# Performance work log

Hardware: AMD Instinct MI355X
Metric: run time of the kernel (lower is better)

The kernel has to match this reference:

```python
import jax, jax.numpy as jnp
import numpy as np

B, LQ, LK, E, HID, H = 4, 1024, 2048, 512, 512, 8


def _ln(x, g, b, eps=1e-5):
    mu = jnp.mean(x, -1, keepdims=True)
    var = jnp.mean((x - mu) ** 2, -1, keepdims=True)
    return (x - mu) * jax.lax.rsqrt(var + eps) * g + b


def _mha(q_in, k_in, v_in, Wq, bq, Wk, bk, Wv, bv, Wo, bo, nheads, q_valid, k_valid):
    # torch nn.MultiheadAttention (batch_first, eval/dropout=0) math
    Bq, Lq, Em = q_in.shape
    Lk = k_in.shape[1]
    hd = Em // nheads
    q = (q_in @ Wq.T + bq).reshape(Bq, Lq, nheads, hd)
    k = (k_in @ Wk.T + bk).reshape(Bq, Lk, nheads, hd)
    v = (v_in @ Wv.T + bv).reshape(Bq, Lk, nheads, hd)
    scale = 1.0 / np.sqrt(hd).astype(np.float32)
    s = jnp.einsum('bqhd,bkhd->bhqk', q, k) * scale
    if k_valid is not None:
        # valid query rows may only attend to valid key columns
        s = jnp.where(k_valid[:, None, None, :], s, jnp.finfo(s.dtype).min)
    w = jax.nn.softmax(s, axis=-1)
    # rows beyond a sample's length are fully masked in the torch nested path
    # (softmax -> NaN, later nan_to_num'd to 0); we zero them directly.
    w = jnp.where(q_valid[:, None, :, None], w, 0.0)
    o = jnp.einsum('bhqk,bkhd->bqhd', w, v).reshape(Bq, Lq, Em)
    return o @ Wo.T + bo, jnp.mean(w, axis=1)  # weights averaged over heads


def setup_inputs() -> dict:
    key = jax.random.key(0)
    ks = jax.random.split(key, 32)
    p = lambda i, shape: 0.02 * jax.random.normal(ks[i], shape, dtype=jnp.float32)
    inp = {
        'queries': jax.random.normal(ks[0], (B, LQ, E), dtype=jnp.float32),
        'keys': jax.random.normal(ks[1], (B, LK, E), dtype=jnp.float32),
        'q_len': jax.random.randint(ks[2], (B,), 1, LQ + 1),
        # cross-attention params
        'cWq': p(3, (E, E)), 'cbq': jnp.zeros((E,)),
        'cWk': p(4, (E, E)), 'cbk': jnp.zeros((E,)),
        'cWv': p(5, (E, E)), 'cbv': jnp.zeros((E,)),
        'cWo': p(6, (E, E)), 'cbo': jnp.zeros((E,)),
        # self-attention params
        'sWq': p(7, (HID, HID)), 'sbq': jnp.zeros((HID,)),
        'sWk': p(8, (HID, HID)), 'sbk': jnp.zeros((HID,)),
        'sWv': p(9, (HID, HID)), 'sbv': jnp.zeros((HID,)),
        'sWo': p(10, (HID, HID)), 'sbo': jnp.zeros((HID,)),
        # ffn + norms
        'Wf': p(11, (HID, E)), 'bf': jnp.zeros((HID,)),
        'g_cross': jnp.ones((E,)), 'b_cross': jnp.zeros((E,)),
        'g_ffn': jnp.ones((HID,)), 'b_ffn': jnp.zeros((HID,)),
        'g_self': jnp.ones((HID,)), 'b_self': jnp.zeros((HID,)),
    }
    return inp


def reference(queries, keys, q_len,
              cWq, cbq, cWk, cbk, cWv, cbv, cWo, cbo,
              sWq, sbq, sWk, sbk, sWv, sbv, sWo, sbo,
              Wf, bf, g_cross, b_cross, g_ffn, b_ffn, g_self, b_self):
    valid = jnp.arange(LQ)[None, :] < q_len[:, None]  # [B, LQ] ragged lengths
    q = jnp.where(valid[..., None], queries, 0.0)     # nested -> padded with 0
    # cross attention: valid rows attend to ALL keys (per the nested mask)
    cross, weights = _mha(q, keys, keys, cWq, cbq, cWk, cbk, cWv, cbv, cWo, cbo,
                          H, valid, None)
    q = _ln(jax.nn.silu(cross + q), g_cross, b_cross)
    f = q @ Wf.T + bf
    q = _ln(jax.nn.silu(q + f), g_ffn, b_ffn)  # q_dim == hidden_dim branch
    q = jnp.where(valid[..., None], q, 0.0)    # torch.nan_to_num on padded rows
    # self attention: valid rows attend only to valid rows of the same sample
    so, _ = _mha(q, q, q, sWq, sbq, sWk, sbk, sWv, sbv, sWo, sbo, H, valid, valid)
    q = _ln(jax.nn.silu(q + so), g_self, b_self)
    q = jnp.where(valid[..., None], q, 0.0)    # padded rows discarded by unbind
    return q, weights
```

## Files before the change

### kernel.cpp

```cpp
#include <hip/hip_runtime.h>

#define BB 4
#define SLQ 1024
#define SLK 2048
#define EE 512
#define HH 8
#define HD 64

typedef unsigned short u16;
typedef __attribute__((ext_vector_type(8))) short s16x8;
typedef __attribute__((ext_vector_type(4))) float f32x4;

__device__ __forceinline__ float bf2f(u16 u) {
  union { unsigned int i; float f; } v; v.i = ((unsigned int)u) << 16; return v.f;
}
__device__ __forceinline__ u16 f2bf(float f) {
  union { float f; unsigned int i; } v; v.f = f;
  unsigned int i = v.i;
  return (u16)((i + 0x7fffu + ((i >> 16) & 1u)) >> 16);
}

__device__ __forceinline__ void async16(const u16* g, u16* l) {
  __builtin_amdgcn_global_load_lds(
      (const __attribute__((address_space(1))) unsigned int*)g,
// ... 9 lines not shown
             const int* __restrict__ qlen)
{
  constexpr int WTM = BM / 2, WTN = BN / 2;
  constexpr int MI = WTM / 16, NI = WTN / 16;
  constexpr int EPAD = WTN + 8;
  constexpr int SM1 = (BM + BN) * 32;
  constexpr int SM2 = (MODE == 0) ? 4 * WTM * EPAD : 0;
  constexpr int SM = (SM1 > SM2) ? SM1 : SM2;

  const int z = blockIdx.z;
  const int tileM = blockIdx.y * BM;
  const int tileN = blockIdx.x * BN;

  if (SKIPQ == 1) { if (tileM >= qlen[z >> 3]) return; }
  if (SKIPQ == 2) { int b = tileM >> 10; if ((tileM & 1023) >= qlen[b]) return; }

  __shared__ __align__(16) u16 smem[SM];
  u16* ldsA = smem;
  u16* ldsB = smem + BM * 32;

  const int t = threadIdx.x;
  const int lane = t & 63;
  const int wave = t >> 6;
  const int waveM = wave >> 1;
  const int waveN = wave & 1;
  const int lm = lane & 15;
  const int kg = lane >> 4;

  const u16* Ab = A + (long)z * sAz + (long)tileM * lda;
  const u16* Bb = Bm + (long)z * sBz + (long)tileN * ldb;

  f32x4 acc[MI][NI];
#pragma unroll
  for (int i = 0; i < MI; ++i)
#pragma unroll
    for (int j = 0; j < NI; ++j) acc[i][j] = (f32x4){0.f, 0.f, 0.f, 0.f};

  for (int kt = 0; kt < K; kt += 32) {
    __syncthreads();
#pragma unroll
    for (int i = 0; i < (BM * 4) / 256; ++i) {
      int c = i * 256 + t;
      async16(Ab + (long)(c >> 2) * lda + kt + (c & 3) * 8, ldsA + (c - lane) * 8);
    }
#pragma unroll
    for (int i = 0; i < (BN * 4) / 256; ++i) {
      int c = i * 256 + t;
      async16(Bb + (long)(c >> 2) * ldb + kt + (c & 3) * 8, ldsB + (c - lane) * 8);
    }
    __syncthreads();

    s16x8 aF[MI], bF[NI];
#pragma unroll
    for (int i = 0; i < MI; ++i)
      aF[i] = *(const s16x8*)&ldsA[(waveM * WTM + i * 16 + lm) * 32 + kg * 8];
#pragma unroll
    for (int j = 0; j < NI; ++j)
      bF[j] = *(const s16x8*)&ldsB[(waveN * WTN + j * 16 + lm) * 32 + kg * 8];
#pragma unroll
    for (int i = 0; i < MI; ++i)
#pragma unroll
      for (int j = 0; j < NI; ++j)
        acc[i][j] = __builtin_amdgcn_mfma_f32_16x16x32_bf16(aF[i], bF[j], acc[i][j], 0, 0, 0);
  }

  if (MODE == 0) {
    u16* ep = smem + wave * (WTM * EPAD);
    __syncthreads();
#pragma unroll
    for (int i = 0; i < MI; ++i)
#pragma unroll
      for (int j = 0; j < NI; ++j) {
        int n = waveN * WTN + j * 16 + lm;
        float bv = bias ? bias[tileN + n] : 0.0f;
#pragma unroll
        for (int r = 0; r < 4; ++r)
          ep[(i * 16 + kg * 4 + r) * EPAD + j * 16 + lm] = f2bf(acc[i][j][r] * alpha + bv);
      }
    const long Crow = (long)z * sCz + (long)(tileM + waveM * WTM) * ldc + tileN + waveN * WTN;
#pragma unroll
    for (int it = 0; it < (WTM * WTN) / 512; ++it) {
      int idx = it * 64 + lane;
      int row = idx / (WTN / 8), seg = idx % (WTN / 8);
      *(uint4*)&C[Crow + (long)row * ldc + seg * 8] =
          *(const uint4*)&ep[row * EPAD + seg * 8];
    }
  } else {
#pragma unroll
    for (int j = 0; j < NI; ++j) {
      int n = tileN + waveN * WTN + j * 16 + lm;
      float bv = bias ? bias[n] : 0.0f;
#pragma unroll
      for (int i = 0; i < MI; ++i) {
#pragma unroll
        for (int r = 0; r < 4; ++r) {
          int m = tileM + waveM * WTM + i * 16 + kg * 4 + r;
          float v = acc[i][j][r] * alpha + bv;
          int b = m / Lsub, l = m - b * Lsub;
          int h = n >> 6, d = n & 63;
          C[(((long)(b * HH + h) * Lsub + l) << 6) + d] = f2bf(v);
        }
      }
    }
  }
}

template<int BM, int BN, int SKIPQ, int NPROJ>
// ... 73 lines not shown
      float bv = bias[n];
#pragma unroll
      for (int i = 0; i < MI; ++i)
#pragma unroll
        for (int r = 0; r < 4; ++r) {
          int m = tileM + waveM * WTM + i * 16 + kg * 4 + r;
          int b = m / Lsub, l = m - b * Lsub;
          int h = n >> 6, d = n & 63;
          C[(((long)(b * HH + h) * Lsub + l) << 6) + d] = f2bf(acc[i][j][r] + bv);
        }
    }
  } else {
    constexpr int PAD = BM + 8;
    const int bb = tileM / Lsub;
    const int l0 = tileM - bb * Lsub;
#pragma unroll
    for (int c = 0; c < BN / 32; ++c) {
      __syncthreads();
#pragma unroll
      for (int j = 0; j < NI; ++j) {
        int nloc = waveN * WTN + j * 16 + lm;
        if (nloc >= c * 32 && nloc < c * 32 + 32) {
          int nl = nloc - c * 32;
          float bv = bias[tileN + nloc];
#pragma unroll
          for (int i = 0; i < MI; ++i)
#pragma unroll
            for (int r = 0; r < 4; ++r) {
              int mm = waveM * WTM + i * 16 + kg * 4 + r;
              smem[nl * PAD + mm] = f2bf(acc[i][j][r] + bv);
            }
        }
      }
      __syncthreads();
#pragma unroll
      for (int v = 0; v < (32 * BM) / (256 * 8); ++v) {
        int idx = v * 256 + t;
        int nl = idx / (BM / 8), m8 = idx % (BM / 8);
        int n = tileN + c * 32 + nl;
        int h = n >> 6, d = n & 63;
        *(uint4*)&C[((long)(bb * HH + h) * HD + d) * Lsub + l0 + m8 * 8] =
            *(const uint4*)&smem[nl * PAD + m8 * 8];
      }
    }
  }
}

__global__ __launch_bounds__(256, 3)
void cross_flash_chunk(const u16* __restrict__ Qc, const u16* __restrict__ Kc,
                       const u16* __restrict__ Vt, u16* __restrict__ Opart,
                       float2* __restrict__ ml, const int* __restrict__ qlen)
{
  const int lin = blockIdx.x;
  const int lid = (lin & 7) * 256 + (lin >> 3);
  const int qt = lid & 15;
  const int bh = (lid >> 4) & 31;
  const int ck = lid >> 9;
  const int b = bh >> 3;
  if (qt * 64 >= qlen[b]) return;

  __shared__ __align__(16) u16 Kt[128 * 72];
  __shared__ __align__(16) u16 Vl[64 * 136];

  const int t = threadIdx.x, lane = t & 63, w = t >> 6;
  const int col = lane & 15, quad = lane >> 4;

  const u16* Qb = Qc + (long)bh * SLQ * HD;
  const u16* Kb = Kc + (long)bh * SLK * HD;
  const u16* Vb = Vt + (long)bh * HD * SLK;

  s16x8 aQ[2];
#pragma unroll
  for (int kk = 0; kk < 2; ++kk)
    aQ[kk] = *(const s16x8*)(Qb + (long)(qt * 64 + w * 16 + col) * HD + kk * 32 + quad * 8);

  f32x4 O[4];
#pragma unroll
  for (int n = 0; n < 4; ++n) O[n] = (f32x4){0.f, 0.f, 0.f, 0.f};
  float mr = -1e30f, lr = 0.f;

  u16* Pw = Kt + w * (16 * 136);

  const int krow = t >> 3, kcol = (t & 7) * 8;
  const int vrow = t >> 4, vcol = (t & 15) * 8;

  uint4 kr0, kr1, kr2, kr3, vr0, vr1, vr2, vr3;
  {
    const int kb = ck * 512;
    kr0 = *(const uint4*)(Kb + (long)(kb + krow) * HD + kcol);
    kr1 = *(const uint4*)(Kb + (long)(kb + krow + 32) * HD + kcol);
    kr2 = *(const uint4*)(Kb + (long)(kb + krow + 64) * HD + kcol);
    kr3 = *(const uint4*)(Kb + (long)(kb + krow + 96) * HD + kcol);
    vr0 = *(const uint4*)(Vb + (long)(vrow) * SLK + kb + vcol);
    vr1 = *(const uint4*)(Vb + (long)(vrow + 16) * SLK + kb + vcol);
    vr2 = *(const uint4*)(Vb + (long)(vrow + 32) * SLK + kb + vcol);
    vr3 = *(const uint4*)(Vb + (long)(vrow + 48) * SLK + kb + vcol);
  }

#pragma unroll
  for (int kt = 0; kt < 4; ++kt) {
    __syncthreads();
    *(uint4*)&Kt[(krow) * 72 + kcol] = kr0;
    *(uint4*)&Kt[(krow + 32) * 72 + kcol] = kr1;
    *(uint4*)&Kt[(krow + 64) * 72 + kcol] = kr2;
    *(uint4*)&Kt[(krow + 96) * 72 + kcol] = kr3;
    *(uint4*)&Vl[(vrow) * 136 + vcol] = vr0;
    *(uint4*)&Vl[(vrow + 16) * 136 + vcol] = vr1;
    *(uint4*)&Vl[(vrow + 32) * 136 + vcol] = vr2;
    *(uint4*)&Vl[(vrow + 48) * 136 + vcol] = vr3;
    if (kt < 3) {
      const int kb = ck * 512 + (kt + 1) * 128;
      kr0 = *(const uint4*)(Kb + (long)(kb + krow) * HD + kcol);
      kr1 = *(const uint4*)(Kb + (long)(kb + krow + 32) * HD + kcol);
      kr2 = *(const uint4*)(Kb + (long)(kb + krow + 64) * HD + kcol);
      kr3 = *(const uint4*)(Kb + (long)(kb + krow + 96) * HD + kcol);
      vr0 = *(const uint4*)(Vb + (long)(vrow) * SLK + kb + vcol);
      vr1 = *(const uint4*)(Vb + (long)(vrow + 16) * SLK + kb + vcol);
      vr2 = *(const uint4*)(Vb + (long)(vrow + 32) * SLK + kb + vcol);
      vr3 = *(const uint4*)(Vb + (long)(vrow + 48) * SLK + kb + vcol);
    }
    __syncthreads();

    f32x4 s[8];
#pragma unroll
    for (int j = 0; j < 8; ++j) s[j] = (f32x4){0.f, 0.f, 0.f, 0.f};
#pragma unroll
    for (int j = 0; j < 8; ++j)
#pragma unroll
      for (int kk = 0; kk < 2; ++kk) {
        s16x8 bK = *(const s16x8*)&Kt[(j * 16 + col) * 72 + kk * 32 + quad * 8];
        s[j] = __builtin_amdgcn_mfma_f32_16x16x32_bf16(bK, aQ[kk], s[j], 0, 0, 0);
      }
#pragma unroll
    for (int j = 0; j < 8; ++j)
#pragma unroll
      for (int r = 0; r < 4; ++r)
        s[j][r] *= 0.125f;

    __syncthreads();

    float mj[8];
#pragma unroll
    for (int j = 0; j < 8; ++j)
      mj[j] = fmaxf(fmaxf(s[j][0], s[j][1]), fmaxf(s[j][2], s[j][3]));
    float tm = fmaxf(fmaxf(fmaxf(mj[0], mj[1]), fmaxf(mj[2], mj[3])),
                     fmaxf(fmaxf(mj[4], mj[5]), fmaxf(mj[6], mj[7])));
    tm = fmaxf(tm, __shfl_xor(tm, 16));
    tm = fmaxf(tm, __shfl_xor(tm, 32));
    float mnew = fmaxf(mr, tm);
    float alpha = __expf(mr - mnew);
    mr = mnew;
    float psj[8];
#pragma unroll
    for (int j = 0; j < 8; ++j) {
      float p0 = __expf(s[j][0] - mnew);
      float p1 = __expf(s[j][1] - mnew);
      float p2 = __expf(s[j][2] - mnew);
      float p3 = __expf(s[j][3] - mnew);
      psj[j] = (p0 + p1) + (p2 + p3);
      unsigned int lo = (unsigned int)f2bf(p0) | ((unsigned int)f2bf(p1) << 16);
      unsigned int hi = (unsigned int)f2bf(p2) | ((unsigned int)f2bf(p3) << 16);
      *(uint2*)&Pw[col * 136 + j * 16 + quad * 4] = (uint2){lo, hi};
    }
    float ps = ((psj[0] + psj[1]) + (psj[2] + psj[3])) +
               ((psj[4] + psj[5]) + (psj[6] + psj[7]));
    ps += __shfl_xor(ps, 16);
    ps += __shfl_xor(ps, 32);
    lr = lr * alpha + ps;

    float a0 = __shfl(alpha, quad * 4 + 0);
    float a1 = __shfl(alpha, quad * 4 + 1);
    float a2 = __shfl(alpha, quad * 4 + 2);
    float a3 = __shfl(alpha, quad * 4 + 3);
#pragma unroll
    for (int n = 0; n < 4; ++n) {
      O[n][0] *= a0; O[n][1] *= a1; O[n][2] *= a2; O[n][3] *= a3;
    }
#pragma unroll
    for (int kk = 0; kk < 4; ++kk) {
      s16x8 aP = *(const s16x8*)&Pw[col * 136 + kk * 32 + quad * 8];
#pragma unroll
      for (int n = 0; n < 4; ++n) {
        s16x8 bV = *(const s16x8*)&Vl[(n * 16 + col) * 136 + kk * 32 + quad * 8];
        O[n] = __builtin_amdgcn_mfma_f32_16x16x32_bf16(aP, bV, O[n], 0, 0, 0);
      }
    }
  }

#pragma unroll
  for (int r = 0; r < 4; ++r) {
    int q = qt * 64 + w * 16 + quad * 4 + r;
    long gq = (long)bh * SLQ + q;
#pragma unroll
    for (int n = 0; n < 4; ++n)
      Opart[(gq * 4 + ck) * 64 + n * 16 + col] = f2bf(O[n][r]);
  }
  if (quad == 0) {
    int q = qt * 64 + w * 16 + col;
    ml[((long)bh * SLQ + q) * 4 + ck] = (float2){mr, lr};
  }
}

__global__ __launch_bounds__(256)
void cross_combine(const u16* __restrict__ Opart, const float2* __restrict__ ml,
                   u16* __restrict__ attn, float2* __restrict__ stat,
                   const int* __restrict__ qlen)
{
  int gr = blockIdx.x * 16 + (threadIdx.x >> 4);
  int bh = gr >> 10, q = gr & 1023;
  int b = bh >> 3, h = bh & 7;
  if (q >= qlen[b]) return;
  int d = (threadIdx.x & 15) * 4;
  long base = (long)gr * 4;
  float M = -1e30f;
#pragma unroll
  for (int c = 0; c < 4; ++c) M = fmaxf(M, ml[base + c].x);
  float L = 0.f;
  float ax = 0.f, ay = 0.f, az = 0.f, aw = 0.f;
#pragma unroll
  for (int c = 0; c < 4; ++c) {
    float2 st = ml[base + c];
    float wgt = __expf(st.x - M);
    L += st.y * wgt;
    const u16* p = Opart + (base + c) * 64 + d;
    ax += bf2f(p[0]) * wgt; ay += bf2f(p[1]) * wgt;
    az += bf2f(p[2]) * wgt; aw += bf2f(p[3]) * wgt;
  }
  if (d == 0) stat[gr] = (float2){M, L};
  float inv = 1.0f / L;
  unsigned int lo = (unsigned int)f2bf(ax * inv) | ((unsigned int)f2bf(ay * inv) << 16);
  unsigned int hi = (unsigned int)f2bf(az * inv) | ((unsigned int)f2bf(aw * inv) << 16);
  *(uint2*)&attn[((long)b * SLQ + q) * EE + h * HD + d] = (uint2){lo, hi};
}

__global__ __launch_bounds__(256, 4)
void wmean_recompute(const u16* __restrict__ Qc, const u16* __restrict__ Kc,
                     const float2* __restrict__ stat, float* __restrict__ outw,
                     const int* __restrict__ qlen)
{
  const int kt = blockIdx.x;
  const int qt = blockIdx.y;
  const int b  = blockIdx.z;
  const int qn = qlen[b];
  const int q0 = qt * 64;
  const int t = threadIdx.x, lane = t & 63, w = t >> 6;
  const int col = lane & 15, quad = lane >> 4;

  float* wr = outw + ((long)b * SLQ + q0) * SLK + kt * 128;

  if (q0 >= qn) {
    float4 z = {0.f, 0.f, 0.f, 0.f};
    for (int i = t; i < 64 * 32; i += 256) {
// ... 29 lines not shown
    *(uint4*)&Kl[(krow + 64) * 72 + kcol] = kr2;
    *(uint4*)&Kl[(krow + 96) * 72 + kcol] = kr3;
    if (h < 7) {
      const u16* Kn = Kbase + (long)(h + 1) * SLK * HD;
      kr0 = *(const uint4*)(Kn + (long)(krow) * HD + kcol);
      kr1 = *(const uint4*)(Kn + (long)(krow + 32) * HD + kcol);
      kr2 = *(const uint4*)(Kn + (long)(krow + 64) * HD + kcol);
      kr3 = *(const uint4*)(Kn + (long)(krow + 96) * HD + kcol);
    }
    const u16* Qb = Qc + ((long)bh * SLQ + qw) * HD;
    s16x8 aQ0 = *(const s16x8*)(Qb + col * HD + quad * 8);
    s16x8 aQ1 = *(const s16x8*)(Qb + col * HD + 32 + quad * 8);
    float m_[4], il_[4];
#pragma unroll
    for (int r = 0; r < 4; ++r) {
      float2 st = stat[(long)bh * SLQ + qw + quad * 4 + r];
      m_[r] = st.x; il_[r] = 0.125f / st.y;
    }
    __syncthreads();

    f32x4 s[8];
#pragma unroll
    for (int j = 0; j < 8; ++j) s[j] = (f32x4){0.f, 0.f, 0.f, 0.f};
#pragma unroll
    for (int j = 0; j < 8; ++j) {
      s16x8 bK0 = *(const s16x8*)&Kl[(j * 16 + col) * 72 + quad * 8];
      s16x8 bK1 = *(const s16x8*)&Kl[(j * 16 + col) * 72 + 32 + quad * 8];
      s[j] = __builtin_amdgcn_mfma_f32_16x16x32_bf16(aQ0, bK0, s[j], 0, 0, 0);
      s[j] = __builtin_amdgcn_mfma_f32_16x16x32_bf16(aQ1, bK1, s[j], 0, 0, 0);
    }
#pragma unroll
    for (int j = 0; j < 8; ++j)
#pragma unroll
      for (int r = 0; r < 4; ++r)
        acc[j][r] += __expf(s[j][r] * 0.125f - m_[r]) * il_[r];
  }

#pragma unroll
  for (int r = 0; r < 4; ++r) {
    int row = w * 16 + quad * 4 + r;
    bool v = (q0 + row) < qn;
#pragma unroll
    for (int j = 0; j < 8; ++j)
      wr[(long)row * SLK + j * 16 + col] = v ? acc[j][r] : 0.f;
  }
}

__global__ __launch_bounds__(256, 3)
void self_flash_chunk(const u16* __restrict__ Qc, const u16* __restrict__ Kc,
                      const u16* __restrict__ Vt, u16* __restrict__ Opart,
                      float2* __restrict__ ml, const int* __restrict__ qlen)
{
  const int lin = blockIdx.x;
  const int lid = (lin & 7) * 256 + (lin >> 3);
  const int qt = lid & 15;
  const int bh = (lid >> 4) & 31;
  const int ck = lid >> 9;
  const int b = bh >> 3;
  const int kmax = qlen[b];
  if (qt * 64 >= kmax || ck * 256 >= kmax) return;

  __shared__ __align__(16) u16 Kt[128 * 72];
  __shared__ __align__(16) u16 Vl[64 * 136];

  const int t = threadIdx.x, lane = t & 63, w = t >> 6;
  const int col = lane & 15, quad = lane >> 4;

  const u16* Qb = Qc + (long)bh * SLQ * HD;
  const u16* Kb = Kc + (long)bh * SLQ * HD;
  const u16* Vb = Vt + (long)bh * HD * SLQ;

  s16x8 aQ[2];
#pragma unroll
  for (int kk = 0; kk < 2; ++kk)
    aQ[kk] = *(const s16x8*)(Qb + (long)(qt * 64 + w * 16 + col) * HD + kk * 32 + quad * 8);

  f32x4 O[4];
#pragma unroll
  for (int n = 0; n < 4; ++n) O[n] = (f32x4){0.f, 0.f, 0.f, 0.f};
  float mr = -1e30f, lr = 0.f;

  u16* Pw = Kt + w * (16 * 136);

  const int krow = t >> 3, kcol = (t & 7) * 8;
  const int vrow = t >> 4, vcol = (t & 15) * 8;

  uint4 kr0, kr1, kr2, kr3, vr0, vr1, vr2, vr3;
  {
    const int kb = ck * 256;
    kr0 = *(const uint4*)(Kb + (long)(kb + krow) * HD + kcol);
    kr1 = *(const uint4*)(Kb + (long)(kb + krow + 32) * HD + kcol);
    kr2 = *(const uint4*)(Kb + (long)(kb + krow + 64) * HD + kcol);
    kr3 = *(const uint4*)(Kb + (long)(kb + krow + 96) * HD + kcol);
    vr0 = *(const uint4*)(Vb + (long)(vrow) * SLQ + kb + vcol);
    vr1 = *(const uint4*)(Vb + (long)(vrow + 16) * SLQ + kb + vcol);
    vr2 = *(const uint4*)(Vb + (long)(vrow + 32) * SLQ + kb + vcol);
    vr3 = *(const uint4*)(Vb + (long)(vrow + 48) * SLQ + kb + vcol);
  }

#pragma unroll
  for (int kt = 0; kt < 2; ++kt) {
    const int k0 = ck * 256 + kt * 128;
    if (k0 >= kmax) break;
    __syncthreads();
    *(uint4*)&Kt[(krow) * 72 + kcol] = kr0;
    *(uint4*)&Kt[(krow + 32) * 72 + kcol] = kr1;
    *(uint4*)&Kt[(krow + 64) * 72 + kcol] = kr2;
    *(uint4*)&Kt[(krow + 96) * 72 + kcol] = kr3;
    *(uint4*)&Vl[(vrow) * 136 + vcol] = vr0;
    *(uint4*)&Vl[(vrow + 16) * 136 + vcol] = vr1;
    *(uint4*)&Vl[(vrow + 32) * 136 + vcol] = vr2;
    *(uint4*)&Vl[(vrow + 48) * 136 + vcol] = vr3;
    if (kt < 1) {
      const int kb = ck * 256 + 128;
      kr0 = *(const uint4*)(Kb + (long)(kb + krow) * HD + kcol);
      kr1 = *(const uint4*)(Kb + (long)(kb + krow + 32) * HD + kcol);
      kr2 = *(const uint4*)(Kb + (long)(kb + krow + 64) * HD + kcol);
      kr3 = *(const uint4*)(Kb + (long)(kb + krow + 96) * HD + kcol);
      vr0 = *(const uint4*)(Vb + (long)(vrow) * SLQ + kb + vcol);
      vr1 = *(const uint4*)(Vb + (long)(vrow + 16) * SLQ + kb + vcol);
      vr2 = *(const uint4*)(Vb + (long)(vrow + 32) * SLQ + kb + vcol);
      vr3 = *(const uint4*)(Vb + (long)(vrow + 48) * SLQ + kb + vcol);
    }
    __syncthreads();

    f32x4 s[8];
#pragma unroll
    for (int j = 0; j < 8; ++j) s[j] = (f32x4){0.f, 0.f, 0.f, 0.f};
#pragma unroll
    for (int j = 0; j < 8; ++j)
#pragma unroll
      for (int kk = 0; kk < 2; ++kk) {
        s16x8 bK = *(const s16x8*)&Kt[(j * 16 + col) * 72 + kk * 32 + quad * 8];
        s[j] = __builtin_amdgcn_mfma_f32_16x16x32_bf16(bK, aQ[kk], s[j], 0, 0, 0);
      }
#pragma unroll
    for (int j = 0; j < 8; ++j)
#pragma unroll
      for (int r = 0; r < 4; ++r) {
        bool ok = (k0 + j * 16 + quad * 4 + r) < kmax;
        s[j][r] = ok ? s[j][r] * 0.125f : -1e30f;
      }

    __syncthreads();

    float mj[8];
#pragma unroll
    for (int j = 0; j < 8; ++j)
      mj[j] = fmaxf(fmaxf(s[j][0], s[j][1]), fmaxf(s[j][2], s[j][3]));
    float tm = fmaxf(fmaxf(fmaxf(mj[0], mj[1]), fmaxf(mj[2], mj[3])),
                     fmaxf(fmaxf(mj[4], mj[5]), fmaxf(mj[6], mj[7])));
    tm = fmaxf(tm, __shfl_xor(tm, 16));
    tm = fmaxf(tm, __shfl_xor(tm, 32));
    float mnew = fmaxf(mr, tm);
    float alpha = __expf(mr - mnew);
    mr = mnew;
    float psj[8];
#pragma unroll
    for (int j = 0; j < 8; ++j) {
      float p0 = __expf(s[j][0] - mnew);
      float p1 = __expf(s[j][1] - mnew);
      float p2 = __expf(s[j][2] - mnew);
      float p3 = __expf(s[j][3] - mnew);
      psj[j] = (p0 + p1) + (p2 + p3);
      unsigned int lo = (unsigned int)f2bf(p0) | ((unsigned int)f2bf(p1) << 16);
      unsigned int hi = (unsigned int)f2bf(p2) | ((unsigned int)f2bf(p3) << 16);
      *(uint2*)&Pw[col * 136 + j * 16 + quad * 4] = (uint2){lo, hi};
    }
    float ps = ((psj[0] + psj[1]) + (psj[2] + psj[3])) +
               ((psj[4] + psj[5]) + (psj[6] + psj[7]));
    ps += __shfl_xor(ps, 16);
    ps += __shfl_xor(ps, 32);
    lr = lr * alpha + ps;

    float a0 = __shfl(alpha, quad * 4 + 0);
    float a1 = __shfl(alpha, quad * 4 + 1);
    float a2 = __shfl(alpha, quad * 4 + 2);
    float a3 = __shfl(alpha, quad * 4 + 3);
#pragma unroll
    for (int n = 0; n < 4; ++n) {
      O[n][0] *= a0; O[n][1] *= a1; O[n][2] *= a2; O[n][3] *= a3;
    }
#pragma unroll
    for (int kk = 0; kk < 4; ++kk) {
      s16x8 aP = *(const s16x8*)&Pw[col * 136 + kk * 32 + quad * 8];
#pragma unroll
      for (int n = 0; n < 4; ++n) {
        s16x8 bV = *(const s16x8*)&Vl[(n * 16 + col) * 136 + kk * 32 + quad * 8];
        O[n] = __builtin_amdgcn_mfma_f32_16x16x32_bf16(aP, bV, O[n], 0, 0, 0);
      }
    }
  }

#pragma unroll
  for (int r = 0; r < 4; ++r) {
    int q = qt * 64 + w * 16 + quad * 4 + r;
    long gq = (long)bh * SLQ + q;
#pragma unroll
    for (int n = 0; n < 4; ++n)
      Opart[(gq * 4 + ck) * 64 + n * 16 + col] = f2bf(O[n][r]);
  }
  if (quad == 0) {
    int q = qt * 64 + w * 16 + col;
    ml[((long)bh * SLQ + q) * 4 + ck] = (float2){mr, lr};
  }
}

__global__ __launch_bounds__(256)
void self_combine(const u16* __restrict__ Opart, const float2* __restrict__ ml,
                  u16* __restrict__ attn, const int* __restrict__ qlen)
{
  int gr = blockIdx.x * 16 + (threadIdx.x >> 4);
  int bh = gr >> 10, q = gr & 1023;
  int b = bh >> 3, h = bh & 7;
  int kmax = qlen[b];
  if (q >= kmax) return;
  int NC = (kmax + 255) >> 8;
  int d = (threadIdx.x & 15) * 4;
  long base = (long)gr * 4;
  float M = -1e30f;
  for (int c = 0; c < NC; ++c) M = fmaxf(M, ml[base + c].x);
  float L = 0.f;
  float ax = 0.f, ay = 0.f, az = 0.f, aw = 0.f;
  for (int c = 0; c < NC; ++c) {
    float2 st = ml[base + c];
    float wgt = __expf(st.x - M);
    L += st.y * wgt;
    const u16* p = Opart + (base + c) * 64 + d;
    ax += bf2f(p[0]) * wgt; ay += bf2f(p[1]) * wgt;
    az += bf2f(p[2]) * wgt; aw += bf2f(p[3]) * wgt;
  }
  float inv = 1.0f / L;
  unsigned int lo = (unsigned int)f2bf(ax * inv) | ((unsigned int)f2bf(ay * inv) << 16);
  unsigned int hi = (unsigned int)f2bf(az * inv) | ((unsigned int)f2bf(aw * inv) << 16);
  *(uint2*)&attn[((long)b * SLQ + q) * EE + h * HD + d] = (uint2){lo, hi};
}

__global__ __launch_bounds__(256)
void cvt_all(const float* __restrict__ queries, const float* __restrict__ keys,
             const int* __restrict__ qlen,
             const float* w0, const float* w1, const float* w2, const float* w3,
             const float* w4, const float* w5, const float* w6, const float* w7,
             const float* w8,
             u16* __restrict__ q0, u16* __restrict__ keysb, u16* __restrict__ Wb) {
  int blk = blockIdx.x;
  int t = threadIdx.x;
  const float* src;
  u16* dst;
  long off;
  bool mask = false;
  int b = 0, q = 0;
  if (blk < 1024) {
    off = (long)blk * 2048 + t * 8;
    int row = (int)(off >> 9);
    b = row >> 10; q = row & 1023;
    mask = true;
    src = queries; dst = q0;
// ... 81 lines not shown
  const float* cWk = (const float*)d_in[5],  *cbk = (const float*)d_in[6];
  const float* cWv = (const float*)d_in[7],  *cbv = (const float*)d_in[8];
  const float* cWo = (const float*)d_in[9],  *cbo = (const float*)d_in[10];
  const float* sWq = (const float*)d_in[11], *sbq = (const float*)d_in[12];
  const float* sWk = (const float*)d_in[13], *sbk = (const float*)d_in[14];
  const float* sWv = (const float*)d_in[15], *sbv = (const float*)d_in[16];
  const float* sWo = (const float*)d_in[17], *sbo = (const float*)d_in[18];
  const float* Wf  = (const float*)d_in[19], *bfb = (const float*)d_in[20];
  const float* g_cross = (const float*)d_in[21], *b_cross = (const float*)d_in[22];
  const float* g_ffn   = (const float*)d_in[23], *b_ffn   = (const float*)d_in[24];
  const float* g_self  = (const float*)d_in[25], *b_self  = (const float*)d_in[26];

  float* out_q = (float*)d_out;
  float* out_w = out_q + (long)BB * SLQ * EE;

  u16* ws = (u16*)d_ws;
  u16* S     = ws;
  u16* Qc    = S   + (long)BB * HH * SLQ * SLK;
  u16* Kc    = Qc  + (long)BB * HH * SLQ * HD;
  u16* Vt    = Kc  + (long)BB * HH * SLK * HD;
  u16* q0    = Vt  + (long)BB * HH * SLK * HD;
  u16* keysb = q0  + (long)BB * SLQ * EE;
  u16* attn  = keysb + (long)BB * SLK * EE;
  u16* proj  = attn + (long)BB * SLQ * EE;
  u16* q1    = proj + (long)BB * SLQ * EE;
  u16* fbuf  = q1  + (long)BB * SLQ * EE;
  u16* q2    = fbuf + (long)BB * SLQ * EE;
  u16* Wb    = q2  + (long)BB * SLQ * EE;
  const long WSLOT = (long)EE * EE;
  u16*    Cpb  = Wb + 9 * WSLOT;
  float2* stat = (float2*)(Cpb + 8388608);

  float2* mlC = (float2*)(S + 33554432);

  u16*    OpS = S;
  float2* mlS = (float2*)(S + 8388608);

  u16* bWq = Wb + 0 * WSLOT; u16* bWk = Wb + 1 * WSLOT; u16* bWv = Wb + 2 * WSLOT;
  u16* bWo = Wb + 3 * WSLOT; u16* bsWq = Wb + 4 * WSLOT; u16* bsWk = Wb + 5 * WSLOT;
  u16* bsWv = Wb + 6 * WSLOT; u16* bsWo = Wb + 7 * WSLOT; u16* bWf = Wb + 8 * WSLOT;

  dim3 blk(256);
  const int MQ = BB * SLQ;
  const int MK = BB * SLK;

  cvt_all<<<dim3(3072 + 9 * 128), blk, 0, stream>>>(
      queries, keys, qlen, cWq, cWk, cWv, cWo, sWq, sWk, sWv, sWo, Wf, q0, keysb, Wb);

  gemm_nt<64, 64, 1, 2><<<dim3(EE / 64, MQ / 64, 1), blk, 0, stream>>>(
      q0, bWq, cbq, Qc, MQ, EE, EE, EE, EE, 0, 0, 0, 0, 1.0f, SLQ, qlen);
  gemm_proj<64, 64, 0, 2><<<dim3(EE / 64, MK / 64, 2), blk, 0, stream>>>(
      keysb, bWk, bWv, nullptr, cbk, cbv, nullptr, Kc, Vt, nullptr, MK, EE, SLK, qlen);

  cross_flash_chunk<<<dim3(2048), blk, 0, stream>>>(Qc, Kc, Vt, Cpb, mlC, qlen);
  cross_combine<<<dim3(2048), blk, 0, stream>>>(Cpb, mlC, attn, stat, qlen);
  wmean_recompute<<<dim3(16, 16, BB), blk, 0, stream>>>(Qc, Kc, stat, out_w, qlen);

  gemm_nt<64, 64, 0, 2><<<dim3(EE / 64, MQ / 64, 1), blk, 0, stream>>>(
      attn, bWo, cbo, proj, MQ, EE, EE, EE, EE, EE, 0, 0, 0, 1.0f, SLQ, qlen);

  silu_ln_kernel<0><<<dim3(MQ), blk, 0, stream>>>(proj, q0, g_cross, b_cross, qlen, q1, 2);

  gemm_nt<64, 64, 0, 2><<<dim3(EE / 64, MQ / 64, 1), blk, 0, stream>>>(
      q1, bWf, bfb, fbuf, MQ, EE, EE, EE, EE, EE, 0, 0, 0, 1.0f, SLQ, qlen);

  silu_ln_kernel<0><<<dim3(MQ), blk, 0, stream>>>(q1, fbuf, g_ffn, b_ffn, qlen, q2, 1);

  gemm_proj<64, 64, 2, 3><<<dim3(EE / 64, MQ / 64, 3), blk, 0, stream>>>(
      q2, bsWq, bsWk, bsWv, sbq, sbk, sbv, Qc, Kc, Vt, MQ, EE, SLQ, qlen);

  self_flash_chunk<<<dim3(2048), blk, 0, stream>>>(Qc, Kc, Vt, OpS, mlS, qlen);
  self_combine<<<dim3(2048), blk, 0, stream>>>(OpS, mlS, attn, qlen);

  gemm_nt<64, 64, 0, 2><<<dim3(EE / 64, MQ / 64, 1), blk, 0, stream>>>(
      attn, bsWo, sbo, proj, MQ, EE, EE, EE, EE, EE, 0, 0, 0, 1.0f, SLQ, qlen);

  silu_ln_kernel<1><<<dim3(MQ), blk, 0, stream>>>(q2, proj, g_self, b_self, qlen, out_q, 1);
}
```

Before: 296.4 us.

## Process two query tiles per flash-attention block to reuse staged K/V tiles

Both the cross and self flash-attention chunk kernels now handle 128 query rows per block (two 64-row groups A and B) instead of 64, so each K/V tile staged into LDS serves twice as many queries and the grid is halved. P gets its own LDS buffer instead of aliasing the K tile, which removes one barrier per tile but raises LDS use and may lower occupancy. The key-tile and group loops are set to unroll 1, which limits register pressure from the doubled accumulators but may cost scheduling freedom. A second group is skipped when it lies beyond the sequence length.

```diff
diff --git a/kernel.cpp b/kernel.cpp
--- a/kernel.cpp
+++ b/kernel.cpp
@@ -85,7 +85,7 @@
 
     s16x8 aF[MI], bF[NI];
 #pragma unroll
-    for (int i = 0; i < MI; ++i)
+  for (int i = 0; i < MI; ++i)
       aF[i] = *(const s16x8*)&ldsA[(waveM * WTM + i * 16 + lm) * 32 + kg * 8];
 #pragma unroll
     for (int j = 0; j < NI; ++j)
@@ -265,15 +265,18 @@
                        float2* __restrict__ ml, const int* __restrict__ qlen)
 {
   const int lin = blockIdx.x;
-  const int lid = (lin & 7) * 256 + (lin >> 3);
-  const int qt = lid & 15;
-  const int bh = (lid >> 4) & 31;
-  const int ck = lid >> 9;
+  const int lid = (lin & 7) * 128 + (lin >> 3);
+  const int qt = lid & 7;
+  const int bh = (lid >> 3) & 31;
+  const int ck = lid >> 8;
   const int b = bh >> 3;
-  if (qt * 64 >= qlen[b]) return;
+  const int qn = qlen[b];
+  if (qt * 128 >= qn) return;
+  const bool doB = (qt * 128 + 64) < qn;
 
   __shared__ __align__(16) u16 Kt[128 * 72];
   __shared__ __align__(16) u16 Vl[64 * 136];
+  __shared__ __align__(16) u16 Pl[4 * 16 * 136];
 
   const int t = threadIdx.x, lane = t & 63, w = t >> 6;
   const int col = lane & 15, quad = lane >> 4;
@@ -282,17 +285,22 @@
   const u16* Kb = Kc + (long)bh * SLK * HD;
   const u16* Vb = Vt + (long)bh * HD * SLK;
 
-  s16x8 aQ[2];
-#pragma unroll
-  for (int kk = 0; kk < 2; ++kk)
-    aQ[kk] = *(const s16x8*)(Qb + (long)(qt * 64 + w * 16 + col) * HD + kk * 32 + quad * 8);
-
-  f32x4 O[4];
-#pragma unroll
-  for (int n = 0; n < 4; ++n) O[n] = (f32x4){0.f, 0.f, 0.f, 0.f};
-  float mr = -1e30f, lr = 0.f;
-
-  u16* Pw = Kt + w * (16 * 136);
+  const int qA = qt * 128 + w * 16 + col;
+  const int qB = qA + 64;
+  s16x8 aQA0 = *(const s16x8*)(Qb + (long)qA * HD + quad * 8);
+  s16x8 aQA1 = *(const s16x8*)(Qb + (long)qA * HD + 32 + quad * 8);
+  s16x8 aQB0 = *(const s16x8*)(Qb + (long)qB * HD + quad * 8);
+  s16x8 aQB1 = *(const s16x8*)(Qb + (long)qB * HD + 32 + quad * 8);
+
+  f32x4 OA[4], OB[4];
+#pragma unroll
+  for (int n = 0; n < 4; ++n) {
+    OA[n] = (f32x4){0.f, 0.f, 0.f, 0.f};
+    OB[n] = (f32x4){0.f, 0.f, 0.f, 0.f};
+  }
+  float mrA = -1e30f, lrA = 0.f, mrB = -1e30f, lrB = 0.f;
+
+  u16* Pw = Pl + w * (16 * 136);
 
   const int krow = t >> 3, kcol = (t & 7) * 8;
   const int vrow = t >> 4, vcol = (t & 15) * 8;
@@ -310,7 +318,7 @@
     vr3 = *(const uint4*)(Vb + (long)(vrow + 48) * SLK + kb + vcol);
   }
 
-#pragma unroll
+#pragma unroll 1
   for (int kt = 0; kt < 4; ++kt) {
     __syncthreads();
     *(uint4*)&Kt[(krow) * 72 + kcol] = kr0;
@@ -334,83 +342,118 @@
     }
     __syncthreads();
 
-    f32x4 s[8];
-#pragma unroll
-    for (int j = 0; j < 8; ++j) s[j] = (f32x4){0.f, 0.f, 0.f, 0.f};
-#pragma unroll
-    for (int j = 0; j < 8; ++j)
-#pragma unroll
-      for (int kk = 0; kk < 2; ++kk) {
-        s16x8 bK = *(const s16x8*)&Kt[(j * 16 + col) * 72 + kk * 32 + quad * 8];
-        s[j] = __builtin_amdgcn_mfma_f32_16x16x32_bf16(bK, aQ[kk], s[j], 0, 0, 0);
-      }
-#pragma unroll
-    for (int j = 0; j < 8; ++j)
-#pragma unroll
-      for (int r = 0; r < 4; ++r)
-        s[j][r] *= 0.125f;
-
-    __syncthreads();
-
-    float mj[8];
-#pragma unroll
-    for (int j = 0; j < 8; ++j)
-      mj[j] = fmaxf(fmaxf(s[j][0], s[j][1]), fmaxf(s[j][2], s[j][3]));
-    float tm = fmaxf(fmaxf(fmaxf(mj[0], mj[1]), fmaxf(mj[2], mj[3])),
-                     fmaxf(fmaxf(mj[4], mj[5]), fmaxf(mj[6], mj[7])));
-    tm = fmaxf(tm, __shfl_xor(tm, 16));
-    tm = fmaxf(tm, __shfl_xor(tm, 32));
-    float mnew = fmaxf(mr, tm);
-    float alpha = __expf(mr - mnew);
-    mr = mnew;
-    float psj[8];
-#pragma unroll
-    for (int j = 0; j < 8; ++j) {
-      float p0 = __expf(s[j][0] - mnew);
-      float p1 = __expf(s[j][1] - mnew);
-      float p2 = __expf(s[j][2] - mnew);
-      float p3 = __expf(s[j][3] - mnew);
-      psj[j] = (p0 + p1) + (p2 + p3);
-      unsigned int lo = (unsigned int)f2bf(p0) | ((unsigned int)f2bf(p1) << 16);
-      unsigned int hi = (unsigned int)f2bf(p2) | ((unsigned int)f2bf(p3) << 16);
-      *(uint2*)&Pw[col * 136 + j * 16 + quad * 4] = (uint2){lo, hi};
-    }
-    float ps = ((psj[0] + psj[1]) + (psj[2] + psj[3])) +
-               ((psj[4] + psj[5]) + (psj[6] + psj[7]));
-    ps += __shfl_xor(ps, 16);
-    ps += __shfl_xor(ps, 32);
-    lr = lr * alpha + ps;
-
-    float a0 = __shfl(alpha, quad * 4 + 0);
-    float a1 = __shfl(alpha, quad * 4 + 1);
-    float a2 = __shfl(alpha, quad * 4 + 2);
-    float a3 = __shfl(alpha, quad * 4 + 3);
-#pragma unroll
-    for (int n = 0; n < 4; ++n) {
-      O[n][0] *= a0; O[n][1] *= a1; O[n][2] *= a2; O[n][3] *= a3;
-    }
-#pragma unroll
-    for (int kk = 0; kk < 4; ++kk) {
-      s16x8 aP = *(const s16x8*)&Pw[col * 136 + kk * 32 + quad * 8];
-#pragma unroll
-      for (int n = 0; n < 4; ++n) {
-        s16x8 bV = *(const s16x8*)&Vl[(n * 16 + col) * 136 + kk * 32 + quad * 8];
-        O[n] = __builtin_amdgcn_mfma_f32_16x16x32_bf16(aP, bV, O[n], 0, 0, 0);
+#pragma unroll 1
+    for (int g = 0; g < 2; ++g) {
+      if (g == 1 && !doB) break;
+      const s16x8 aQ0 = (g == 0) ? aQA0 : aQB0;
+      const s16x8 aQ1 = (g == 0) ? aQA1 : aQB1;
+      float mr = (g == 0) ? mrA : mrB;
+      float lr = (g == 0) ? lrA : lrB;
+
+      f32x4 s[8];
+#pragma unroll
+      for (int j = 0; j < 8; ++j) s[j] = (f32x4){0.f, 0.f, 0.f, 0.f};
+#pragma unroll
+      for (int j = 0; j < 8; ++j) {
+        s16x8 bK0 = *(const s16x8*)&Kt[(j * 16 + col) * 72 + quad * 8];
+        s16x8 bK1 = *(const s16x8*)&Kt[(j * 16 + col) * 72 + 32 + quad * 8];
+        s[j] = __builtin_amdgcn_mfma_f32_16x16x32_bf16(bK0, aQ0, s[j], 0, 0, 0);
+        s[j] = __builtin_amdgcn_mfma_f32_16x16x32_bf16(bK1, aQ1, s[j], 0, 0, 0);
+      }
+#pragma unroll
+      for (int j = 0; j < 8; ++j)
+#pragma unroll
+        for (int r = 0; r < 4; ++r)
+          s[j][r] *= 0.125f;
+
+      float mj[8];
+#pragma unroll
+      for (int j = 0; j < 8; ++j)
+        mj[j] = fmaxf(fmaxf(s[j][0], s[j][1]), fmaxf(s[j][2], s[j][3]));
+      float tm = fmaxf(fmaxf(fmaxf(mj[0], mj[1]), fmaxf(mj[2], mj[3])),
+                       fmaxf(fmaxf(mj[4], mj[5]), fmaxf(mj[6], mj[7])));
+      tm = fmaxf(tm, __shfl_xor(tm, 16));
+      tm = fmaxf(tm, __shfl_xor(tm, 32));
+      float mnew = fmaxf(mr, tm);
+      float alpha = __expf(mr - mnew);
+      mr = mnew;
+      float psj[8];
+#pragma unroll
+      for (int j = 0; j < 8; ++j) {
+        float p0 = __expf(s[j][0] - mnew);
+        float p1 = __expf(s[j][1] - mnew);
+        float p2 = __expf(s[j][2] - mnew);
+        float p3 = __expf(s[j][3] - mnew);
+        psj[j] = (p0 + p1) + (p2 + p3);
+        unsigned int lo = (unsigned int)f2bf(p0) | ((unsigned int)f2bf(p1) << 16);
+        unsigned int hi = (unsigned int)f2bf(p2) | ((unsigned int)f2bf(p3) << 16);
+        *(uint2*)&Pw[col * 136 + j * 16 + quad * 4] = (uint2){lo, hi};
+      }
+      float ps = ((psj[0] + psj[1]) + (psj[2] + psj[3])) +
+                 ((psj[4] + psj[5]) + (psj[6] + psj[7]));
+      ps += __shfl_xor(ps, 16);
+      ps += __shfl_xor(ps, 32);
+      lr = lr * alpha + ps;
+
+      float a0 = __shfl(alpha, quad * 4 + 0);
+      float a1 = __shfl(alpha, quad * 4 + 1);
+      float a2 = __shfl(alpha, quad * 4 + 2);
+      float a3 = __shfl(alpha, quad * 4 + 3);
+      if (g == 0) {
+#pragma unroll
+        for (int n = 0; n < 4; ++n) {
+          OA[n][0] *= a0; OA[n][1] *= a1; OA[n][2] *= a2; OA[n][3] *= a3;
+        }
+#pragma unroll
+        for (int kk = 0; kk < 4; ++kk) {
+          s16x8 aP = *(const s16x8*)&Pw[col * 136 + kk * 32 + quad * 8];
+#pragma unroll
+          for (int n = 0; n < 4; ++n) {
+            s16x8 bV = *(const s16x8*)&Vl[(n * 16 + col) * 136 + kk * 32 + quad * 8];
+            OA[n] = __builtin_amdgcn_mfma_f32_16x16x32_bf16(aP, bV, OA[n], 0, 0, 0);
+          }
+        }
+        mrA = mr; lrA = lr;
+      } else {
+#pragma unroll
+        for (int n = 0; n < 4; ++n) {
+          OB[n][0] *= a0; OB[n][1] *= a1; OB[n][2] *= a2; OB[n][3] *= a3;
+        }
+#pragma unroll
+        for (int kk = 0; kk < 4; ++kk) {
+          s16x8 aP = *(const s16x8*)&Pw[col * 136 + kk * 32 + quad * 8];
+#pragma unroll
+          for (int n = 0; n < 4; ++n) {
+            s16x8 bV = *(const s16x8*)&Vl[(n * 16 + col) * 136 + kk * 32 + quad * 8];
+            OB[n] = __builtin_amdgcn_mfma_f32_16x16x32_bf16(aP, bV, OB[n], 0, 0, 0);
+          }
+        }
+        mrB = mr; lrB = lr;
       }
     }
   }
 
 #pragma unroll
   for (int r = 0; r < 4; ++r) {
-    int q = qt * 64 + w * 16 + quad * 4 + r;
+    int q = qt * 128 + w * 16 + quad * 4 + r;
     long gq = (long)bh * SLQ + q;
 #pragma unroll
     for (int n = 0; n < 4; ++n)
-      Opart[(gq * 4 + ck) * 64 + n * 16 + col] = f2bf(O[n][r]);
-  }
-  if (quad == 0) {
-    int q = qt * 64 + w * 16 + col;
-    ml[((long)bh * SLQ + q) * 4 + ck] = (float2){mr, lr};
+      Opart[(gq * 4 + ck) * 64 + n * 16 + col] = f2bf(OA[n][r]);
+  }
+  if (quad == 0)
+    ml[((long)bh * SLQ + qA) * 4 + ck] = (float2){mrA, lrA};
+  if (doB) {
+#pragma unroll
+    for (int r = 0; r < 4; ++r) {
+      int q = qt * 128 + 64 + w * 16 + quad * 4 + r;
+      long gq = (long)bh * SLQ + q;
+#pragma unroll
+      for (int n = 0; n < 4; ++n)
+        Opart[(gq * 4 + ck) * 64 + n * 16 + col] = f2bf(OB[n][r]);
+    }
+    if (quad == 0)
+      ml[((long)bh * SLQ + qB) * 4 + ck] = (float2){mrB, lrB};
   }
 }
 
@@ -546,16 +589,18 @@
                       float2* __restrict__ ml, const int* __restrict__ qlen)
 {
   const int lin = blockIdx.x;
-  const int lid = (lin & 7) * 256 + (lin >> 3);
-  const int qt = lid & 15;
-  const int bh = (lid >> 4) & 31;
-  const int ck = lid >> 9;
+  const int lid = (lin & 7) * 128 + (lin >> 3);
+  const int qt = lid & 7;
+  const int bh = (lid >> 3) & 31;
+  const int ck = lid >> 8;
   const int b = bh >> 3;
   const int kmax = qlen[b];
-  if (qt * 64 >= kmax || ck * 256 >= kmax) return;
+  if (qt * 128 >= kmax || ck * 256 >= kmax) return;
+  const bool doB = (qt * 128 + 64) < kmax;
 
   __shared__ __align__(16) u16 Kt[128 * 72];
   __shared__ __align__(16) u16 Vl[64 * 136];
+  __shared__ __align__(16) u16 Pl[4 * 16 * 136];
 
   const int t = threadIdx.x, lane = t & 63, w = t >> 6;
   const int col = lane & 15, quad = lane >> 4;
@@ -564,17 +609,22 @@
   const u16* Kb = Kc + (long)bh * SLQ * HD;
   const u16* Vb = Vt + (long)bh * HD * SLQ;
 
-  s16x8 aQ[2];
-#pragma unroll
-  for (int kk = 0; kk < 2; ++kk)
-    aQ[kk] = *(const s16x8*)(Qb + (long)(qt * 64 + w * 16 + col) * HD + kk * 32 + quad * 8);
-
-  f32x4 O[4];
-#pragma unroll
-  for (int n = 0; n < 4; ++n) O[n] = (f32x4){0.f, 0.f, 0.f, 0.f};
-  float mr = -1e30f, lr = 0.f;
-
-  u16* Pw = Kt + w * (16 * 136);
+  const int qA = qt * 128 + w * 16 + col;
+  const int qB = qA + 64;
+  s16x8 aQA0 = *(const s16x8*)(Qb + (long)qA * HD + quad * 8);
+  s16x8 aQA1 = *(const s16x8*)(Qb + (long)qA * HD + 32 + quad * 8);
+  s16x8 aQB0 = *(const s16x8*)(Qb + (long)qB * HD + quad * 8);
+  s16x8 aQB1 = *(const s16x8*)(Qb + (long)qB * HD + 32 + quad * 8);
+
+  f32x4 OA[4], OB[4];
+#pragma unroll
+  for (int n = 0; n < 4; ++n) {
+    OA[n] = (f32x4){0.f, 0.f, 0.f, 0.f};
+    OB[n] = (f32x4){0.f, 0.f, 0.f, 0.f};
+  }
+  float mrA = -1e30f, lrA = 0.f, mrB = -1e30f, lrB = 0.f;
+
+  u16* Pw = Pl + w * (16 * 136);
 
   const int krow = t >> 3, kcol = (t & 7) * 8;
   const int vrow = t >> 4, vcol = (t & 15) * 8;
@@ -592,7 +642,7 @@
     vr3 = *(const uint4*)(Vb + (long)(vrow + 48) * SLQ + kb + vcol);
   }
 
-#pragma unroll
+#pragma unroll 1
   for (int kt = 0; kt < 2; ++kt) {
     const int k0 = ck * 256 + kt * 128;
     if (k0 >= kmax) break;
@@ -618,85 +668,120 @@
     }
     __syncthreads();
 
-    f32x4 s[8];
-#pragma unroll
-    for (int j = 0; j < 8; ++j) s[j] = (f32x4){0.f, 0.f, 0.f, 0.f};
-#pragma unroll
-    for (int j = 0; j < 8; ++j)
-#pragma unroll
-      for (int kk = 0; kk < 2; ++kk) {
-        s16x8 bK = *(const s16x8*)&Kt[(j * 16 + col) * 72 + kk * 32 + quad * 8];
-        s[j] = __builtin_amdgcn_mfma_f32_16x16x32_bf16(bK, aQ[kk], s[j], 0, 0, 0);
-      }
-#pragma unroll
-    for (int j = 0; j < 8; ++j)
-#pragma unroll
-      for (int r = 0; r < 4; ++r) {
-        bool ok = (k0 + j * 16 + quad * 4 + r) < kmax;
-        s[j][r] = ok ? s[j][r] * 0.125f : -1e30f;
-      }
-
-    __syncthreads();
-
-    float mj[8];
-#pragma unroll
-    for (int j = 0; j < 8; ++j)
-      mj[j] = fmaxf(fmaxf(s[j][0], s[j][1]), fmaxf(s[j][2], s[j][3]));
-    float tm = fmaxf(fmaxf(fmaxf(mj[0], mj[1]), fmaxf(mj[2], mj[3])),
-                     fmaxf(fmaxf(mj[4], mj[5]), fmaxf(mj[6], mj[7])));
-    tm = fmaxf(tm, __shfl_xor(tm, 16));
-    tm = fmaxf(tm, __shfl_xor(tm, 32));
-    float mnew = fmaxf(mr, tm);
-    float alpha = __expf(mr - mnew);
-    mr = mnew;
-    float psj[8];
-#pragma unroll
-    for (int j = 0; j < 8; ++j) {
-      float p0 = __expf(s[j][0] - mnew);
-      float p1 = __expf(s[j][1] - mnew);
-      float p2 = __expf(s[j][2] - mnew);
-      float p3 = __expf(s[j][3] - mnew);
-      psj[j] = (p0 + p1) + (p2 + p3);
-      unsigned int lo = (unsigned int)f2bf(p0) | ((unsigned int)f2bf(p1) << 16);
-      unsigned int hi = (unsigned int)f2bf(p2) | ((unsigned int)f2bf(p3) << 16);
-      *(uint2*)&Pw[col * 136 + j * 16 + quad * 4] = (uint2){lo, hi};
-    }
-    float ps = ((psj[0] + psj[1]) + (psj[2] + psj[3])) +
-               ((psj[4] + psj[5]) + (psj[6] + psj[7]));
-    ps += __shfl_xor(ps, 16);
-    ps += __shfl_xor(ps, 32);
-    lr = lr * alpha + ps;
-
-    float a0 = __shfl(alpha, quad * 4 + 0);
-    float a1 = __shfl(alpha, quad * 4 + 1);
-    float a2 = __shfl(alpha, quad * 4 + 2);
-    float a3 = __shfl(alpha, quad * 4 + 3);
-#pragma unroll
-    for (int n = 0; n < 4; ++n) {
-      O[n][0] *= a0; O[n][1] *= a1; O[n][2] *= a2; O[n][3] *= a3;
-    }
-#pragma unroll
-    for (int kk = 0; kk < 4; ++kk) {
-      s16x8 aP = *(const s16x8*)&Pw[col * 136 + kk * 32 + quad * 8];
-#pragma unroll
-      for (int n = 0; n < 4; ++n) {
-        s16x8 bV = *(const s16x8*)&Vl[(n * 16 + col) * 136 + kk * 32 + quad * 8];
-        O[n] = __builtin_amdgcn_mfma_f32_16x16x32_bf16(aP, bV, O[n], 0, 0, 0);
+#pragma unroll 1
+    for (int g = 0; g < 2; ++g) {
+      if (g == 1 && !doB) break;
+      const s16x8 aQ0 = (g == 0) ? aQA0 : aQB0;
+      const s16x8 aQ1 = (g == 0) ? aQA1 : aQB1;
+      float mr = (g == 0) ? mrA : mrB;
+      float lr = (g == 0) ? lrA : lrB;
+
+      f32x4 s[8];
+#pragma unroll
+      for (int j = 0; j < 8; ++j) s[j] = (f32x4){0.f, 0.f, 0.f, 0.f};
+#pragma unroll
+      for (int j = 0; j < 8; ++j) {
+        s16x8 bK0 = *(const s16x8*)&Kt[(j * 16 + col) * 72 + quad * 8];
+        s16x8 bK1 = *(const s16x8*)&Kt[(j * 16 + col) * 72 + 32 + quad * 8];
+        s[j] = __builtin_amdgcn_mfma_f32_16x16x32_bf16(bK0, aQ0, s[j], 0, 0, 0);
+        s[j] = __builtin_amdgcn_mfma_f32_16x16x32_bf16(bK1, aQ1, s[j], 0, 0, 0);
+      }
+#pragma unroll
+      for (int j = 0; j < 8; ++j)
+#pragma unroll
+        for (int r = 0; r < 4; ++r) {
+          bool ok = (k0 + j * 16 + quad * 4 + r) < kmax;
+          s[j][r] = ok ? s[j][r] * 0.125f : -1e30f;
+        }
+
+      float mj[8];
+#pragma unroll
+      for (int j = 0; j < 8; ++j)
+        mj[j] = fmaxf(fmaxf(s[j][0], s[j][1]), fmaxf(s[j][2], s[j][3]));
+      float tm = fmaxf(fmaxf(fmaxf(mj[0], mj[1]), fmaxf(mj[2], mj[3])),
+                       fmaxf(fmaxf(mj[4], mj[5]), fmaxf(mj[6], mj[7])));
+      tm = fmaxf(tm, __shfl_xor(tm, 16));
+      tm = fmaxf(tm, __shfl_xor(tm, 32));
+      float mnew = fmaxf(mr, tm);
+      float alpha = __expf(mr - mnew);
+      mr = mnew;
+      float psj[8];
+#pragma unroll
+      for (int j = 0; j < 8; ++j) {
+        float p0 = __expf(s[j][0] - mnew);
+        float p1 = __expf(s[j][1] - mnew);
+        float p2 = __expf(s[j][2] - mnew);
+        float p3 = __expf(s[j][3] - mnew);
+        psj[j] = (p0 + p1) + (p2 + p3);
+        unsigned int lo = (unsigned int)f2bf(p0) | ((unsigned int)f2bf(p1) << 16);
+        unsigned int hi = (unsigned int)f2bf(p2) | ((unsigned int)f2bf(p3) << 16);
+        *(uint2*)&Pw[col * 136 + j * 16 + quad * 4] = (uint2){lo, hi};
+      }
+      float ps = ((psj[0] + psj[1]) + (psj[2] + psj[3])) +
+                 ((psj[4] + psj[5]) + (psj[6] + psj[7]));
+      ps += __shfl_xor(ps, 16);
+      ps += __shfl_xor(ps, 32);
+      lr = lr * alpha + ps;
+
+      float a0 = __shfl(alpha, quad * 4 + 0);
+      float a1 = __shfl(alpha, quad * 4 + 1);
+      float a2 = __shfl(alpha, quad * 4 + 2);
+      float a3 = __shfl(alpha, quad * 4 + 3);
+      if (g == 0) {
+#pragma unroll
+        for (int n = 0; n < 4; ++n) {
+          OA[n][0] *= a0; OA[n][1] *= a1; OA[n][2] *= a2; OA[n][3] *= a3;
+        }
+#pragma unroll
+        for (int kk = 0; kk < 4; ++kk) {
+          s16x8 aP = *(const s16x8*)&Pw[col * 136 + kk * 32 + quad * 8];
+#pragma unroll
+          for (int n = 0; n < 4; ++n) {
+            s16x8 bV = *(const s16x8*)&Vl[(n * 16 + col) * 136 + kk * 32 + quad * 8];
+            OA[n] = __builtin_amdgcn_mfma_f32_16x16x32_bf16(aP, bV, OA[n], 0, 0, 0);
+          }
+        }
+        mrA = mr; lrA = lr;
+      } else {
+#pragma unroll
+        for (int n = 0; n < 4; ++n) {
+          OB[n][0] *= a0; OB[n][1] *= a1; OB[n][2] *= a2; OB[n][3] *= a3;
+        }
+#pragma unroll
+        for (int kk = 0; kk < 4; ++kk) {
+          s16x8 aP = *(const s16x8*)&Pw[col * 136 + kk * 32 + quad * 8];
+#pragma unroll
+          for (int n = 0; n < 4; ++n) {
+            s16x8 bV = *(const s16x8*)&Vl[(n * 16 + col) * 136 + kk * 32 + quad * 8];
+            OB[n] = __builtin_amdgcn_mfma_f32_16x16x32_bf16(aP, bV, OB[n], 0, 0, 0);
+          }
+        }
+        mrB = mr; lrB = lr;
       }
     }
   }
 
 #pragma unroll
   for (int r = 0; r < 4; ++r) {
-    int q = qt * 64 + w * 16 + quad * 4 + r;
+    int q = qt * 128 + w * 16 + quad * 4 + r;
     long gq = (long)bh * SLQ + q;
 #pragma unroll
     for (int n = 0; n < 4; ++n)
-      Opart[(gq * 4 + ck) * 64 + n * 16 + col] = f2bf(O[n][r]);
-  }
-  if (quad == 0) {
-    int q = qt * 64 + w * 16 + col;
-    ml[((long)bh * SLQ + q) * 4 + ck] = (float2){mr, lr};
+      Opart[(gq * 4 + ck) * 64 + n * 16 + col] = f2bf(OA[n][r]);
+  }
+  if (quad == 0)
+    ml[((long)bh * SLQ + qA) * 4 + ck] = (float2){mrA, lrA};
+  if (doB) {
+#pragma unroll
+    for (int r = 0; r < 4; ++r) {
+      int q = qt * 128 + 64 + w * 16 + quad * 4 + r;
+      long gq = (long)bh * SLQ + q;
+#pragma unroll
+      for (int n = 0; n < 4; ++n)
+        Opart[(gq * 4 + ck) * 64 + n * 16 + col] = f2bf(OB[n][r]);
+    }
+    if (quad == 0)
+      ml[((long)bh * SLQ + qB) * 4 + ck] = (float2){mrB, lrB};
   }
 }
 
@@ -884,7 +969,7 @@
   gemm_proj<64, 64, 0, 2><<<dim3(EE / 64, MK / 64, 2), blk, 0, stream>>>(
       keysb, bWk, bWv, nullptr, cbk, cbv, nullptr, Kc, Vt, nullptr, MK, EE, SLK, qlen);
 
-  cross_flash_chunk<<<dim3(2048), blk, 0, stream>>>(Qc, Kc, Vt, Cpb, mlC, qlen);
+  cross_flash_chunk<<<dim3(1024), blk, 0, stream>>>(Qc, Kc, Vt, Cpb, mlC, qlen);
   cross_combine<<<dim3(2048), blk, 0, stream>>>(Cpb, mlC, attn, stat, qlen);
   wmean_recompute<<<dim3(16, 16, BB), blk, 0, stream>>>(Qc, Kc, stat, out_w, qlen);
 
@@ -901,7 +986,7 @@
   gemm_proj<64, 64, 2, 3><<<dim3(EE / 64, MQ / 64, 3), blk, 0, stream>>>(
       q2, bsWq, bsWk, bsWv, sbq, sbk, sbv, Qc, Kc, Vt, MQ, EE, SLQ, qlen);
 
-  self_flash_chunk<<<dim3(2048), blk, 0, stream>>>(Qc, Kc, Vt, OpS, mlS, qlen);
+  self_flash_chunk<<<dim3(1024), blk, 0, stream>>>(Qc, Kc, Vt, OpS, mlS, qlen);
   self_combine<<<dim3(2048), blk, 0, stream>>>(OpS, mlS, attn, qlen);
 
   gemm_nt<64, 64, 0, 2><<<dim3(EE / 64, MQ / 64, 1), blk, 0, stream>>>(
```

After: 367.2 us. 23.9% more time.
